# Kernel optimization log

Measured on AMD Instinct MI355X. Metric: run time of the kernel, lower is better.

The kernel has to match this reference:

```python
import jax, jax.numpy as jnp
import numpy as np

NUM_HEADS = 16
DIM = 1024
HARMONICS = 32
B, L = 2, 2048


def holo_linear(x, basis, phase, amp):
    # x: [B,L,in]; basis: [H,in] (L2-normalized rows); phase/amp: [out,H]
    # Original builds complex(res,0) * amp*exp(i*phase) and takes real of sum
    # over harmonics -> sum_h res_h * amp[o,h]*cos(phase[o,h]).
    resonance = jnp.einsum('bli,hi->blh', x, basis)        # [B,L,H]
    w = amp * jnp.cos(phase)                               # [out,H]
    return jnp.einsum('blh,oh->blo', resonance, w)         # [B,L,out]


def setup_inputs() -> dict:
    key = jax.random.key(0)
    ks = jax.random.split(key, 13)
    two_pi = 2.0 * np.pi

    def make_proj(k0, k1):
        basis = jax.random.normal(k0, (HARMONICS, DIM), dtype=jnp.float32)
        basis = basis / jnp.linalg.norm(basis, axis=1, keepdims=True)
        phase = jax.random.normal(k1, (DIM, HARMONICS), dtype=jnp.float32) * two_pi
        amp = jnp.ones((DIM, HARMONICS), dtype=jnp.float32) / HARMONICS
        return basis, phase, amp

    x = jax.random.normal(ks[0], (B, L, DIM), dtype=jnp.float32)
    bq, pq, aq = make_proj(ks[1], ks[2])
    bk, pk, ak = make_proj(ks[3], ks[4])
    bv, pv, av = make_proj(ks[5], ks[6])
    bo, po, ao = make_proj(ks[7], ks[8])
    return {
        'x': x,
        'basis_q': bq, 'phase_q': pq, 'amp_q': aq,
        'basis_k': bk, 'phase_k': pk, 'amp_k': ak,
        'basis_v': bv, 'phase_v': pv, 'amp_v': av,
        'basis_o': bo, 'phase_o': po, 'amp_o': ao,
    }


def reference(x, basis_q, phase_q, amp_q, basis_k, phase_k, amp_k,
              basis_v, phase_v, amp_v, basis_o, phase_o, amp_o):
    Bsz, Ls, C = x.shape
    head_dim = C // NUM_HEADS
    scale = head_dim ** (-0.5)

    def split_heads(t):  # [B,L,C] -> [B,H,L,hd]
        return t.reshape(Bsz, Ls, NUM_HEADS, head_dim).transpose(0, 2, 1, 3)

    q = split_heads(holo_linear(x, basis_q, phase_q, amp_q))
    k = split_heads(holo_linear(x, basis_k, phase_k, amp_k))
    v = split_heads(holo_linear(x, basis_v, phase_v, amp_v))

    attn = jnp.einsum('bhqd,bhkd->bhqk', q, k) * scale      # [B,H,L,L]
    attn = jax.nn.softmax(attn, axis=-1)
    out = jnp.einsum('bhqk,bhkd->bhqd', attn, v)            # [B,H,L,hd]
    out = out.transpose(0, 2, 1, 3).reshape(Bsz, Ls, C)
    return holo_linear(out, basis_o, phase_o, amp_o)
```

## Files before the change

### kernel.cpp

```cpp
#include <hip/hip_runtime.h>
#include <hip/hip_bf16.h>
#include <cstdint>
#include <cstddef>

#define NH   16
#define HD   64
#define CD   1024
#define HARM 32
#define BSZ  2
#define LSEQ 2048
#define NROW (BSZ*LSEQ)

typedef __attribute__((ext_vector_type(8))) short short8;
typedef __attribute__((ext_vector_type(16))) float float16v;

__device__ inline ushort bf16u(float f) {
    __hip_bfloat16 h = __float2bfloat16(f);
    return *(ushort*)&h;
}
__device__ inline float ubf(ushort u) {
    return __uint_as_float((unsigned)u << 16);
}
__device__ inline unsigned pk2(float a, float b) {
    return (unsigned)bf16u(a) | ((unsigned)bf16u(b) << 16);
}
__device__ inline int crow(int r, int half) { return (r & 3) + 8 * (r >> 2) + 4 * half; }

union S8U { short8 v; uint2 u[2]; };

__device__ inline short8 pk_frag(const unsigned* pk, int cc) {
    S8U o;
    o.u[0] = make_uint2(pk[4 * cc + 0], pk[4 * cc + 1]);
    o.u[1] = make_uint2(pk[4 * cc + 2], pk[4 * cc + 3]);
    return o.v;
}

__global__ void prep_kern(const float* __restrict__ bq, const float* __restrict__ bk,
                          const float* __restrict__ bv, const float* __restrict__ bo,
                          const float* __restrict__ pq, const float* __restrict__ aq,
                          const float* __restrict__ pk, const float* __restrict__ ak,
                          const float* __restrict__ pv, const float* __restrict__ av,
                          const float* __restrict__ po, const float* __restrict__ ao,
                          ushort* __restrict__ bF, ushort* __restrict__ wqkvF,
                          ushort* __restrict__ wobF) {
    const float QSCALE = 0.125f * 1.44269504088896340736f;
    unsigned tid = blockIdx.x * 256 + threadIdx.x;
    if (tid < 16384) {
        unsigned l31 = tid & 31, h = (tid >> 5) & 1, kc = (tid >> 6) & 63, proj = tid >> 12;
        const float* bp = (proj == 0) ? bq : (proj == 1) ? bk : (proj == 2) ? bv : bo;
        const float* s = bp + (size_t)l31 * CD + kc * 16;
        unsigned o0 = (proj == 3) ? h * 4 : h * 8;
        unsigned o1 = o0 + ((proj == 3) ? 8 : 4);
        float4 f0 = *(const float4*)(s + o0), f1 = *(const float4*)(s + o1);
        S8U o;
        o.u[0] = make_uint2(pk2(f0.x, f0.y), pk2(f0.z, f0.w));
        o.u[1] = make_uint2(pk2(f1.x, f1.y), pk2(f1.z, f1.w));
        *(short8*)(bF + (size_t)tid * 8) = o.v;
        return;
    }
    if (tid < 28672) {
        unsigned i = tid - 16384;
        unsigned l31 = i & 31, h = (i >> 5) & 1, kc2 = (i >> 6) & 1;
        unsigned ntp = (i >> 7) & 31, proj = i >> 12;
        const float* ph = (proj == 0) ? pq : (proj == 1) ? pk : pv;
        const float* am = (proj == 0) ? aq : (proj == 1) ? ak : av;
        float sc = (proj == 0) ? QSCALE : 1.0f;
        size_t s = (size_t)(ntp * 32 + l31) * HARM + kc2 * 16 + h * 4;
        float4 p0 = *(const float4*)(ph + s), p1 = *(const float4*)(ph + s + 8);
        float4 a0 = *(const float4*)(am + s), a1 = *(const float4*)(am + s + 8);
        S8U o;
        o.u[0] = make_uint2(pk2(a0.x * cosf(p0.x) * sc, a0.y * cosf(p0.y) * sc),
                            pk2(a0.z * cosf(p0.z) * sc, a0.w * cosf(p0.w) * sc));
        o.u[1] = make_uint2(pk2(a1.x * cosf(p1.x) * sc, a1.y * cosf(p1.y) * sc),
                            pk2(a1.z * cosf(p1.z) * sc, a1.w * cosf(p1.w) * sc));
        *(short8*)(wqkvF + (size_t)i * 8) = o.v;
        return;
    }
    {
        unsigned i = tid - 28672;
        unsigned l31 = i & 31, h = (i >> 5) & 1, kc2 = (i >> 6) & 1, nt = i >> 7;
        size_t s = (size_t)(nt * 32 + l31) * HARM + kc2 * 16 + h * 4;
        float4 p0 = *(const float4*)(po + s), p1 = *(const float4*)(po + s + 8);
        float4 a0 = *(const float4*)(ao + s), a1 = *(const float4*)(ao + s + 8);
        S8U o;
        o.u[0] = make_uint2(pk2(a0.x * cosf(p0.x), a0.y * cosf(p0.y)),
                            pk2(a0.z * cosf(p0.z), a0.w * cosf(p0.w)));
        o.u[1] = make_uint2(pk2(a1.x * cosf(p1.x), a1.y * cosf(p1.y)),
                            pk2(a1.z * cosf(p1.z), a1.w * cosf(p1.w)));
        *(short8*)(wobF + (size_t)i * 8) = o.v;
    }
}

__global__ __launch_bounds__(256) void res_part_kern(const float* __restrict__ x,
                                                     const ushort* __restrict__ bF,
                                                     float* __restrict__ respart) {
    __shared__ ushort xs[32 * 256];
    __shared__ float red[4 * 16 * 64];
    const int t = threadIdx.x, wave = t >> 6, lane = t & 63;
    const int l31 = lane & 31, h = lane >> 5;
    const int kseg = blockIdx.x & 3, rg = blockIdx.x >> 2;
    const int n0 = rg * 32;

#pragma unroll
    for (int i = 0; i < 8; i++) {
        int idx = i * 256 + t, row = idx >> 6, c4 = idx & 63;
        float4 v = *(const float4*)(x + (size_t)(n0 + row) * CD + kseg * 256 + c4 * 4);
        int chunk = (c4 >> 1) ^ (row & 15), sub = c4 & 1;
        *(ushort4*)(&xs[row * 256 + chunk * 8 + sub * 4]) =
            make_ushort4(bf16u(v.x), bf16u(v.y), bf16u(v.z), bf16u(v.w));
    }
    __syncthreads();

    float16v resC[3] = {};
#pragma unroll
    for (int kci = 0; kci < 4; kci++) {
        int c = wave * 8 + kci * 2 + h;
        short8 bx = *(const short8*)(&xs[l31 * 256 + (c ^ (l31 & 15)) * 8]);
        int kcg = kseg * 16 + wave * 4 + kci;
#pragma unroll
        for (int p = 0; p < 3; p++) {
            short8 a = *(const short8*)(bF + ((size_t)((p * 64 + kcg) * 2 + h) * 32 + l31) * 8);
            resC[p] = __builtin_amdgcn_mfma_f32_32x32x16_bf16(a, bx, resC[p], 0, 0, 0);
        }
    }
    float* outb = respart + ((size_t)(kseg * 128 + rg) * 3) * 1024;
    for (int p = 0; p < 3; p++) {
        __syncthreads();
#pragma unroll
        for (int r = 0; r < 16; r++) red[wave * 1024 + r * 64 + lane] = resC[p][r];
        __syncthreads();
#pragma unroll
        for (int i = 0; i < 4; i++) {
            int e = i * 256 + t;
            outb[p * 1024 + e] = (red[e] + red[1024 + e]) + (red[2048 + e] + red[3072 + e]);
        }
    }
}

__global__ __launch_bounds__(256) void rp_kern(const float* __restrict__ respart,
                                               unsigned* __restrict__ rfbuf) {
    const int tid = blockIdx.x * 256 + threadIdx.x;
    const int rest = tid / 384, u = tid % 384;
    const int p = u >> 7, cc = (u >> 6) & 1, lane = u & 63;

    const float* base = respart + ((size_t)rest * 3 + p) * 1024 + cc * 512 + lane;
    unsigned w[4];
#pragma unroll
    for (int q = 0; q < 4; q++) {
        const float* pa = base + (2 * q) * 64;
        const float* pb = pa + 64;
        float a = (pa[0] + pa[393216]) + (pa[2 * 393216] + pa[3 * 393216]);
        float bv_ = (pb[0] + pb[393216]) + (pb[2 * 393216] + pb[3 * 393216]);
        w[q] = pk2(a, bv_);
    }
    *(uint4*)(rfbuf + (size_t)rest * 1536 + ((p * 2 + cc) * 64 + lane) * 4) =
        make_uint4(w[0], w[1], w[2], w[3]);
}

__global__ __launch_bounds__(256) void qkv_kern(const unsigned* __restrict__ rfbuf,
                                                const ushort* __restrict__ wqkvF,
                                                ushort* __restrict__ qtile,
                                                ushort* __restrict__ ktile,
                                                ushort* __restrict__ vtile) {
    const int t = threadIdx.x, wave = t >> 6, lane = t & 63;
    const int l31 = lane & 31, h = lane >> 5;
    const int ntg = blockIdx.x % 24, rest = blockIdx.x / 24;
    const int b = rest >> 6, l0q = rest & 63;
    const int nt = ntg * 4 + wave;
    const int proj = nt >> 5, ntp = nt & 31;
    const int head = ntp >> 1, sub = ntp & 1;
    const int kblk = l0q >> 1, mtk = l0q & 1;

    const unsigned* rb = rfbuf + (size_t)rest * 1536 + ((proj * 2) * 64 + lane) * 4;
    uint4 q0 = *(const uint4*)(rb);
    uint4 q1 = *(const uint4*)(rb + 256);
    S8U r0, r1;
    r0.u[0] = make_uint2(q0.x, q0.y); r0.u[1] = make_uint2(q0.z, q0.w);
    r1.u[0] = make_uint2(q1.x, q1.y); r1.u[1] = make_uint2(q1.z, q1.w);

    const ushort* wp = wqkvF + ((size_t)(proj * 32 + ntp) * 4) * 256;
    short8 wf0 = *(const short8*)(wp + (size_t)h * 256 + l31 * 8);
    short8 wf1 = *(const short8*)(wp + (size_t)(2 + h) * 256 + l31 * 8);
    float16v c = {};
    if (proj < 2) {
        c = __builtin_amdgcn_mfma_f32_32x32x16_bf16(wf0, r0.v, c, 0, 0, 0);
        c = __builtin_amdgcn_mfma_f32_32x32x16_bf16(wf1, r1.v, c, 0, 0, 0);
    } else {
        c = __builtin_amdgcn_mfma_f32_32x32x16_bf16(r0.v, wf0, c, 0, 0, 0);
        c = __builtin_amdgcn_mfma_f32_32x32x16_bf16(r1.v, wf1, c, 0, 0, 0);
    }
    unsigned pkc[8];
#pragma unroll
    for (int j = 0; j < 8; j++) pkc[j] = pk2(c[2 * j], c[2 * j + 1]);

    if (proj == 0) {
        ushort* base = qtile + (((size_t)(b * NH + head) * 64 + l0q)) * 2048;
#pragma unroll
        for (int cc = 0; cc < 2; cc++)
            *(short8*)(base + (sub * 2 + cc) * 512 + h * 256 + l31 * 8) =
                pk_frag(pkc, cc);
    } else if (proj == 1) {
        ushort* base = ktile + ((size_t)(b * NH + head) * 32 + kblk) * 4096 + mtk * 2048;
#pragma unroll
        for (int cc = 0; cc < 2; cc++)
            *(short8*)(base + (sub * 2 + cc) * 512 + h * 256 + l31 * 8) =
                pk_frag(pkc, cc);
    } else {
        ushort* base = vtile + ((size_t)(b * NH + head) * 32 + kblk) * 4096 + sub * 2048;
#pragma unroll
        for (int cc = 0; cc < 2; cc++)
            *(short8*)(base + (mtk * 2 + cc) * 512 + h * 256 + l31 * 8) =
                pk_frag(pkc, cc);
    }
}

__global__ __launch_bounds__(256, 2) void flash8(const ushort* __restrict__ qtile,
                                                 const ushort* __restrict__ ktile,
                                                 const ushort* __restrict__ vtile,
                                                 ushort* __restrict__ Opart,
                                                 float* __restrict__ lbuf) {
    __shared__ ushort kb[2][4096];
    __shared__ ushort vb[2][4096];
    const int t = threadIdx.x;
    const int wave = t >> 6, lane = t & 63;
    const int l31 = lane & 31, h = lane >> 5;
    const int d = blockIdx.x;
    const int logical = (d & 7) * 128 + (d >> 3);
    const int bh = logical >> 5;
    const int inner = logical & 31;
    const int ksp = inner >> 4;
    const int qt = (inner & 15) * 4 + wave;
    const int fo = h * 256 + l31 * 8;
    const int so = t * 8;

    const ushort* qtb = qtile + ((size_t)bh * 64 + qt) * 2048;
    short8 qf[4];
#pragma unroll
    for (int kc = 0; kc < 4; kc++) qf[kc] = *(const short8*)(qtb + kc * 512 + fo);

    const ushort* ktb = ktile + (size_t)bh * 32 * 4096;
    const ushort* vtb = vtile + (size_t)bh * 32 * 4096;
    const int k0 = ksp * 16;

    {
        const ushort* ks = ktb + (size_t)k0 * 4096;
        const ushort* vs = vtb + (size_t)k0 * 4096;
        short8 a0 = *(const short8*)(ks + so);
        short8 a1 = *(const short8*)(ks + 2048 + so);
        short8 b0 = *(const short8*)(vs + so);
        short8 b1 = *(const short8*)(vs + 2048 + so);
        *(short8*)(kb[0] + so) = a0; *(short8*)(kb[0] + 2048 + so) = a1;
        *(short8*)(vb[0] + so) = b0; *(short8*)(vb[0] + 2048 + so) = b1;
    }
    __syncthreads();

    S8U ones;
    ones.u[0] = make_uint2(0x3F803F80u, 0x3F803F80u);
    ones.u[1] = make_uint2(0x3F803F80u, 0x3F803F80u);

    float16v O0 = {}, O1 = {}, La = {};

#pragma unroll
    for (int it = 0; it < 16; it++) {
        const int cur = it & 1, nxt = cur ^ 1;

        short8 a0, a1, b0, b1;
        if (it < 15) {
            const ushort* ks = ktb + (size_t)(k0 + it + 1) * 4096;
            const ushort* vs = vtb + (size_t)(k0 + it + 1) * 4096;
            a0 = *(const short8*)(ks + so);
            a1 = *(const short8*)(ks + 2048 + so);
            b0 = *(const short8*)(vs + so);
            b1 = *(const short8*)(vs + 2048 + so);
        }

        short8 kf[2][4];
#pragma unroll
        for (int mt = 0; mt < 2; mt++)
#pragma unroll
            for (int kc = 0; kc < 4; kc++)
                kf[mt][kc] = *(const short8*)(kb[cur] + mt * 2048 + kc * 512 + fo);
        float16v s0 = {}, s1 = {};
#pragma unroll
        for (int kc = 0; kc < 4; kc++) {
            s0 = __builtin_amdgcn_mfma_f32_32x32x16_bf16(kf[0][kc], qf[kc], s0, 0, 0, 0);
            s1 = __builtin_amdgcn_mfma_f32_32x32x16_bf16(kf[1][kc], qf[kc], s1, 0, 0, 0);
        }
        short8 vf[2][4];
#pragma unroll
        for (int mt = 0; mt < 2; mt++)
#pragma unroll
            for (int kc = 0; kc < 4; kc++)
                vf[mt][kc] = *(const short8*)(vb[cur] + mt * 2048 + kc * 512 + fo);

        unsigned pk0[8], pk1[8];
#pragma unroll
        for (int j2 = 0; j2 < 8; j2++) {
            pk0[j2] = pk2(__builtin_amdgcn_exp2f(s0[2 * j2]),
                          __builtin_amdgcn_exp2f(s0[2 * j2 + 1]));
            pk1[j2] = pk2(__builtin_amdgcn_exp2f(s1[2 * j2]),
                          __builtin_amdgcn_exp2f(s1[2 * j2 + 1]));
        }
#pragma unroll
        for (int kc = 0; kc < 4; kc++) {
            const unsigned* pkm = (kc < 2) ? pk0 : pk1;
            short8 bf = pk_frag(pkm, kc & 1);
            La = __builtin_amdgcn_mfma_f32_32x32x16_bf16(ones.v, bf, La, 0, 0, 0);
            O0 = __builtin_amdgcn_mfma_f32_32x32x16_bf16(vf[0][kc], bf, O0, 0, 0, 0);
            O1 = __builtin_amdgcn_mfma_f32_32x32x16_bf16(vf[1][kc], bf, O1, 0, 0, 0);
        }

        if (it < 15) {
            *(short8*)(kb[nxt] + so) = a0; *(short8*)(kb[nxt] + 2048 + so) = a1;
            *(short8*)(vb[nxt] + so) = b0; *(short8*)(vb[nxt] + 2048 + so) = b1;
        }
        __syncthreads();
    }

    if (h == 0) lbuf[(size_t)ksp * 65536 + bh * 2048 + qt * 32 + l31] = La[0];
    ushort* ob = Opart + (size_t)ksp * 4194304 + ((size_t)bh * 64 + qt) * 2048;
#pragma unroll
    for (int mt = 0; mt < 2; mt++) {
        float16v Ov = mt ? O1 : O0;
        unsigned pkO[8];
#pragma unroll
        for (int j2 = 0; j2 < 8; j2++) pkO[j2] = pk2(Ov[2 * j2], Ov[2 * j2 + 1]);
#pragma unroll
        for (int cc = 0; cc < 2; cc++)
            *(short8*)(ob + ((mt * 2 + cc) * 2 + h) * 256 + l31 * 8) =
                pk_frag(pkO, cc);
    }
}

__global__ __launch_bounds__(256) void back1_kern(const ushort* __restrict__ Opart,
                                                  const float* __restrict__ lbuf,
                                                  const ushort* __restrict__ bF,
                                                  float* __restrict__ respart2) {
    __shared__ float red[4 * 16 * 64];
    const int t = threadIdx.x, wave = t >> 6, lane = t & 63;
    const int l31 = lane & 31, h = lane >> 5;
    const int hq = blockIdx.x & 3, rg = blockIdx.x >> 2;
    const int b = rg >> 6, qt = rg & 63;
    const int hd = hq * 4 + wave, bh = b * NH + hd;

    float lb = lbuf[(size_t)bh * 2048 + qt * 32 + l31] +
               lbuf[(size_t)65536 + (size_t)bh * 2048 + qt * 32 + l31];
    float invl = 1.0f / lb;
    const ushort* ob0 = Opart + ((size_t)bh * 64 + qt) * 2048;
    const ushort* ob1 = ob0 + 4194304;

    float16v c = {};
#pragma unroll
    for (int kc = 0; kc < 4; kc++) {
        short8 o0 = *(const short8*)(ob0 + (kc * 2 + h) * 256 + l31 * 8);
        short8 o1 = *(const short8*)(ob1 + (kc * 2 + h) * 256 + l31 * 8);
        float av[8];
#pragma unroll
        for (int e = 0; e < 8; e++)
            av[e] = (ubf((ushort)o0[e]) + ubf((ushort)o1[e])) * invl;
        S8U bn;
        bn.u[0] = make_uint2(pk2(av[0], av[1]), pk2(av[2], av[3]));
        bn.u[1] = make_uint2(pk2(av[4], av[5]), pk2(av[6], av[7]));
        int kcg = hd * 4 + kc;
        short8 a = *(const short8*)(bF + ((size_t)((3 * 64 + kcg) * 2 + h) * 32 + l31) * 8);
        c = __builtin_amdgcn_mfma_f32_32x32x16_bf16(a, bn.v, c, 0, 0, 0);
    }
#pragma unroll
    for (int r = 0; r < 16; r++) red[wave * 1024 + r * 64 + lane] = c[r];
    __syncthreads();
#pragma unroll
    for (int i = 0; i < 4; i++) {
        int e = i * 256 + t;
        respart2[((size_t)hq * 128 + rg) * 1024 + e] =
            (red[e] + red[1024 + e]) + (red[2048 + e] + red[3072 + e]);
    }
}

__global__ __launch_bounds__(256) void back2_kern(const float* __restrict__ respart2,
                                                  const ushort* __restrict__ wobF,
                                                  float* __restrict__ out) {
    const int t = threadIdx.x, wave = t >> 6, lane = t & 63;
    const int l31 = lane & 31, h = lane >> 5;
    const int ng = blockIdx.x & 7, rg = blockIdx.x >> 3;

    float cf[16];
#pragma unroll
    for (int r = 0; r < 16; r++) {
        const float* pp = respart2 + r * 64 + lane;
        cf[r] = (pp[(size_t)rg * 1024] + pp[(size_t)(128 + rg) * 1024]) +
                (pp[(size_t)(256 + rg) * 1024] + pp[(size_t)(384 + rg) * 1024]);
    }
    unsigned pkr[8];
#pragma unroll
    for (int j = 0; j < 8; j++) pkr[j] = pk2(cf[2 * j], cf[2 * j + 1]);
    short8 a0 = pk_frag(pkr, 0);
    short8 a1 = pk_frag(pkr, 1);

    int nt = ng * 4 + wave;
    const ushort* wp = wobF + (size_t)nt * 1024;
    short8 wf0 = *(const short8*)(wp + (size_t)h * 256 + l31 * 8);
    short8 wf1 = *(const short8*)(wp + (size_t)(2 + h) * 256 + l31 * 8);
    float16v co = {};
    co = __builtin_amdgcn_mfma_f32_32x32x16_bf16(a0, wf0, co, 0, 0, 0);
    co = __builtin_amdgcn_mfma_f32_32x32x16_bf16(a1, wf1, co, 0, 0, 0);
#pragma unroll
    for (int r = 0; r < 16; r++) {
        int row = rg * 32 + crow(r, h);
        out[(size_t)row * CD + nt * 32 + l31] = co[r];
    }
}

extern "C" void kernel_launch(void* const* d_in, const int* in_sizes, int n_in,
                              void* d_out, int out_size, void* d_ws, size_t ws_size,
                              hipStream_t stream) {
    const float* x  = (const float*)d_in[0];
    const float* bq = (const float*)d_in[1];
    const float* pq = (const float*)d_in[2];
    const float* aq = (const float*)d_in[3];
    const float* bk = (const float*)d_in[4];
    const float* pk = (const float*)d_in[5];
    const float* ak = (const float*)d_in[6];
    const float* bv = (const float*)d_in[7];
    const float* pv = (const float*)d_in[8];
    const float* av = (const float*)d_in[9];
    const float* bo = (const float*)d_in[10];
    const float* po = (const float*)d_in[11];
    const float* ao = (const float*)d_in[12];

    char* ws = (char*)d_ws;
    ushort* bF      = (ushort*)(ws + 0);
    ushort* wqkvF   = (ushort*)(ws + 262144);
    ushort* wobF    = (ushort*)(ws + 458752);
    ushort* qtile   = (ushort*)(ws + 524288);
    ushort* ktile   = (ushort*)(ws + 8912896);
    ushort* vtile   = (ushort*)(ws + 17301504);
    ushort* Opart   = (ushort*)(ws + 25690112);
    float*  lbuf    = (float*)(ws + 42467328);
    float*  respart = (float*)(ws + 42991616);
    float*  respart2= (float*)(ws + 524288);
    unsigned* rfbuf = (unsigned*)(ws + 25690112);

    prep_kern<<<128, 256, 0, stream>>>(bq, bk, bv, bo, pq, aq, pk, ak, pv, av,
                                       po, ao, bF, wqkvF, wobF);
    res_part_kern<<<512, 256, 0, stream>>>(x, bF, respart);
    rp_kern<<<192, 256, 0, stream>>>(respart, rfbuf);
    qkv_kern<<<3072, 256, 0, stream>>>(rfbuf, wqkvF, qtile, ktile, vtile);
    flash8<<<BSZ * NH * 32, 256, 0, stream>>>(qtile, ktile, vtile, Opart, lbuf);
    back1_kern<<<512, 256, 0, stream>>>(Opart, lbuf, bF, respart2);
    back2_kern<<<1024, 256, 0, stream>>>(respart2, wobF, (float*)d_out);
}
```

Measured before the change: 158.0 us.

## Process two query tiles per wave in flash kernel to reuse K/V fragments

Each wave now handles two 32-row query tiles instead of one. The K and V fragments loaded from LDS are reused across both, and the grid is halved to 512 blocks. This is meant to cut LDS reads and K/V global loads per unit of work. In exchange it raises register pressure with doubled accumulators, which could reduce occupancy under launch_bounds(256,2), and it leaves fewer blocks to fill the CUs.

```diff
diff --git a/kernel.cpp b/kernel.cpp
--- a/kernel.cpp
+++ b/kernel.cpp
@@ -225,18 +225,22 @@
     const int wave = t >> 6, lane = t & 63;
     const int l31 = lane & 31, h = lane >> 5;
     const int d = blockIdx.x;
-    const int logical = (d & 7) * 128 + (d >> 3);
-    const int bh = logical >> 5;
-    const int inner = logical & 31;
-    const int ksp = inner >> 4;
-    const int qt = (inner & 15) * 4 + wave;
+    const int logical = (d & 7) * 64 + (d >> 3);
+    const int bh = logical >> 4;
+    const int inner = logical & 15;
+    const int ksp = inner >> 3;
+    const int qtg = inner & 7;
+    const int qt0 = qtg * 8 + wave * 2;
     const int fo = h * 256 + l31 * 8;
     const int so = t * 8;
 
-    const ushort* qtb = qtile + ((size_t)bh * 64 + qt) * 2048;
-    short8 qf[4];
-#pragma unroll
-    for (int kc = 0; kc < 4; kc++) qf[kc] = *(const short8*)(qtb + kc * 512 + fo);
+    const ushort* qtb = qtile + ((size_t)bh * 64 + qt0) * 2048;
+    short8 qfa[4], qfb[4];
+#pragma unroll
+    for (int kc = 0; kc < 4; kc++) {
+        qfa[kc] = *(const short8*)(qtb + kc * 512 + fo);
+        qfb[kc] = *(const short8*)(qtb + 2048 + kc * 512 + fo);
+    }
 
     const ushort* ktb = ktile + (size_t)bh * 32 * 4096;
     const ushort* vtb = vtile + (size_t)bh * 32 * 4096;
@@ -258,7 +262,8 @@
     ones.u[0] = make_uint2(0x3F803F80u, 0x3F803F80u);
     ones.u[1] = make_uint2(0x3F803F80u, 0x3F803F80u);
 
-    float16v O0 = {}, O1 = {}, La = {};
+    float16v O0a = {}, O1a = {}, Laa = {};
+    float16v O0b = {}, O1b = {}, Lab = {};
 
 #pragma unroll
     for (int it = 0; it < 16; it++) {
@@ -280,11 +285,13 @@
 #pragma unroll
             for (int kc = 0; kc < 4; kc++)
                 kf[mt][kc] = *(const short8*)(kb[cur] + mt * 2048 + kc * 512 + fo);
-        float16v s0 = {}, s1 = {};
+        float16v s0a = {}, s1a = {}, s0b = {}, s1b = {};
 #pragma unroll
         for (int kc = 0; kc < 4; kc++) {
-            s0 = __builtin_amdgcn_mfma_f32_32x32x16_bf16(kf[0][kc], qf[kc], s0, 0, 0, 0);
-            s1 = __builtin_amdgcn_mfma_f32_32x32x16_bf16(kf[1][kc], qf[kc], s1, 0, 0, 0);
+            s0a = __builtin_amdgcn_mfma_f32_32x32x16_bf16(kf[0][kc], qfa[kc], s0a, 0, 0, 0);
+            s1a = __builtin_amdgcn_mfma_f32_32x32x16_bf16(kf[1][kc], qfa[kc], s1a, 0, 0, 0);
+            s0b = __builtin_amdgcn_mfma_f32_32x32x16_bf16(kf[0][kc], qfb[kc], s0b, 0, 0, 0);
+            s1b = __builtin_amdgcn_mfma_f32_32x32x16_bf16(kf[1][kc], qfb[kc], s1b, 0, 0, 0);
         }
         short8 vf[2][4];
 #pragma unroll
@@ -293,21 +300,30 @@
             for (int kc = 0; kc < 4; kc++)
                 vf[mt][kc] = *(const short8*)(vb[cur] + mt * 2048 + kc * 512 + fo);
 
-        unsigned pk0[8], pk1[8];
+        unsigned pk0a[8], pk1a[8], pk0b[8], pk1b[8];
 #pragma unroll
         for (int j2 = 0; j2 < 8; j2++) {
-            pk0[j2] = pk2(__builtin_amdgcn_exp2f(s0[2 * j2]),
-                          __builtin_amdgcn_exp2f(s0[2 * j2 + 1]));
-            pk1[j2] = pk2(__builtin_amdgcn_exp2f(s1[2 * j2]),
-                          __builtin_amdgcn_exp2f(s1[2 * j2 + 1]));
+            pk0a[j2] = pk2(__builtin_amdgcn_exp2f(s0a[2 * j2]),
+                           __builtin_amdgcn_exp2f(s0a[2 * j2 + 1]));
+            pk1a[j2] = pk2(__builtin_amdgcn_exp2f(s1a[2 * j2]),
+                           __builtin_amdgcn_exp2f(s1a[2 * j2 + 1]));
+            pk0b[j2] = pk2(__builtin_amdgcn_exp2f(s0b[2 * j2]),
+                           __builtin_amdgcn_exp2f(s0b[2 * j2 + 1]));
+            pk1b[j2] = pk2(__builtin_amdgcn_exp2f(s1b[2 * j2]),
+                           __builtin_amdgcn_exp2f(s1b[2 * j2 + 1]));
         }
 #pragma unroll
         for (int kc = 0; kc < 4; kc++) {
-            const unsigned* pkm = (kc < 2) ? pk0 : pk1;
-            short8 bf = pk_frag(pkm, kc & 1);
-            La = __builtin_amdgcn_mfma_f32_32x32x16_bf16(ones.v, bf, La, 0, 0, 0);
-            O0 = __builtin_amdgcn_mfma_f32_32x32x16_bf16(vf[0][kc], bf, O0, 0, 0, 0);
-            O1 = __builtin_amdgcn_mfma_f32_32x32x16_bf16(vf[1][kc], bf, O1, 0, 0, 0);
+            const unsigned* pma = (kc < 2) ? pk0a : pk1a;
+            const unsigned* pmb = (kc < 2) ? pk0b : pk1b;
+            short8 bfa = pk_frag(pma, kc & 1);
+            short8 bfb = pk_frag(pmb, kc & 1);
+            Laa = __builtin_amdgcn_mfma_f32_32x32x16_bf16(ones.v, bfa, Laa, 0, 0, 0);
+            O0a = __builtin_amdgcn_mfma_f32_32x32x16_bf16(vf[0][kc], bfa, O0a, 0, 0, 0);
+            O1a = __builtin_amdgcn_mfma_f32_32x32x16_bf16(vf[1][kc], bfa, O1a, 0, 0, 0);
+            Lab = __builtin_amdgcn_mfma_f32_32x32x16_bf16(ones.v, bfb, Lab, 0, 0, 0);
+            O0b = __builtin_amdgcn_mfma_f32_32x32x16_bf16(vf[0][kc], bfb, O0b, 0, 0, 0);
+            O1b = __builtin_amdgcn_mfma_f32_32x32x16_bf16(vf[1][kc], bfb, O1b, 0, 0, 0);
         }
 
         if (it < 15) {
@@ -317,18 +333,24 @@
         __syncthreads();
     }
 
-    if (h == 0) lbuf[(size_t)ksp * 65536 + bh * 2048 + qt * 32 + l31] = La[0];
-    ushort* ob = Opart + (size_t)ksp * 4194304 + ((size_t)bh * 64 + qt) * 2048;
-#pragma unroll
-    for (int mt = 0; mt < 2; mt++) {
-        float16v Ov = mt ? O1 : O0;
-        unsigned pkO[8];
-#pragma unroll
-        for (int j2 = 0; j2 < 8; j2++) pkO[j2] = pk2(Ov[2 * j2], Ov[2 * j2 + 1]);
-#pragma unroll
-        for (int cc = 0; cc < 2; cc++)
-            *(short8*)(ob + ((mt * 2 + cc) * 2 + h) * 256 + l31 * 8) =
-                pk_frag(pkO, cc);
+    if (h == 0) {
+        lbuf[(size_t)ksp * 65536 + bh * 2048 + qt0 * 32 + l31] = Laa[0];
+        lbuf[(size_t)ksp * 65536 + bh * 2048 + (qt0 + 1) * 32 + l31] = Lab[0];
+    }
+#pragma unroll
+    for (int j = 0; j < 2; j++) {
+        ushort* ob = Opart + (size_t)ksp * 4194304 + ((size_t)bh * 64 + qt0 + j) * 2048;
+#pragma unroll
+        for (int mt = 0; mt < 2; mt++) {
+            float16v Ov = j ? (mt ? O1b : O0b) : (mt ? O1a : O0a);
+            unsigned pkO[8];
+#pragma unroll
+            for (int j2 = 0; j2 < 8; j2++) pkO[j2] = pk2(Ov[2 * j2], Ov[2 * j2 + 1]);
+#pragma unroll
+            for (int cc = 0; cc < 2; cc++)
+                *(short8*)(ob + ((mt * 2 + cc) * 2 + h) * 256 + l31 * 8) =
+                    pk_frag(pkO, cc);
+        }
     }
 }
 
@@ -445,7 +467,7 @@
     res_part_kern<<<512, 256, 0, stream>>>(x, bF, respart);
     rp_kern<<<192, 256, 0, stream>>>(respart, rfbuf);
     qkv_kern<<<3072, 256, 0, stream>>>(rfbuf, wqkvF, qtile, ktile, vtile);
-    flash8<<<BSZ * NH * 32, 256, 0, stream>>>(qtile, ktile, vtile, Opart, lbuf);
+    flash8<<<512, 256, 0, stream>>>(qtile, ktile, vtile, Opart, lbuf);
     back1_kern<<<512, 256, 0, stream>>>(Opart, lbuf, bF, respart2);
     back2_kern<<<1024, 256, 0, stream>>>(respart2, wobF, (float*)d_out);
 }
```

After: 151.6 us, median of 2. -4.0%, faster.

## Software-pipeline QK^T one tile ahead of exp and PV in attention loop

Applied to the files above, without the earlier changes.

Restructures the attention inner loop so the S = K·Q MFMA for the next key tile is computed while the exp/pack and P·V MFMAs of the current tile proceed. K is prefetched two tiles ahead and V one tile ahead, with separate double-buffer indices for each. This is meant to hide the exp2/pack latency behind matrix-core work and overlap more independent MFMA chains. In exchange it adds a prologue, holds two S accumulator sets in registers (more VGPR pressure), and changes the buffer-reuse pattern around the barriers.

```diff
diff --git a/kernel.cpp b/kernel.cpp
--- a/kernel.cpp
+++ b/kernel.cpp
@@ -258,49 +258,80 @@
     ones.u[0] = make_uint2(0x3F803F80u, 0x3F803F80u);
     ones.u[1] = make_uint2(0x3F803F80u, 0x3F803F80u);
 
+    float16v sS[2][2];
+    {
+        short8 ka0, ka1;
+        {
+            const ushort* ks = ktb + (size_t)(k0 + 1) * 4096;
+            ka0 = *(const short8*)(ks + so);
+            ka1 = *(const short8*)(ks + 2048 + so);
+        }
+        short8 kf[2][4];
+#pragma unroll
+        for (int mt = 0; mt < 2; mt++)
+#pragma unroll
+            for (int kc = 0; kc < 4; kc++)
+                kf[mt][kc] = *(const short8*)(kb[0] + mt * 2048 + kc * 512 + fo);
+        sS[0][0] = (float16v){};
+        sS[0][1] = (float16v){};
+#pragma unroll
+        for (int kc = 0; kc < 4; kc++) {
+            sS[0][0] = __builtin_amdgcn_mfma_f32_32x32x16_bf16(kf[0][kc], qf[kc], sS[0][0], 0, 0, 0);
+            sS[0][1] = __builtin_amdgcn_mfma_f32_32x32x16_bf16(kf[1][kc], qf[kc], sS[0][1], 0, 0, 0);
+        }
+        *(short8*)(kb[1] + so) = ka0; *(short8*)(kb[1] + 2048 + so) = ka1;
+    }
+    __syncthreads();
+
     float16v O0 = {}, O1 = {}, La = {};
 
 #pragma unroll
     for (int it = 0; it < 16; it++) {
-        const int cur = it & 1, nxt = cur ^ 1;
-
-        short8 a0, a1, b0, b1;
+        const int pc = it & 1, pn = pc ^ 1;
+
+        short8 ka0, ka1, va0, va1;
+        if (it < 14) {
+            const ushort* ks = ktb + (size_t)(k0 + it + 2) * 4096;
+            ka0 = *(const short8*)(ks + so);
+            ka1 = *(const short8*)(ks + 2048 + so);
+        }
         if (it < 15) {
-            const ushort* ks = ktb + (size_t)(k0 + it + 1) * 4096;
             const ushort* vs = vtb + (size_t)(k0 + it + 1) * 4096;
-            a0 = *(const short8*)(ks + so);
-            a1 = *(const short8*)(ks + 2048 + so);
-            b0 = *(const short8*)(vs + so);
-            b1 = *(const short8*)(vs + 2048 + so);
-        }
-
-        short8 kf[2][4];
+            va0 = *(const short8*)(vs + so);
+            va1 = *(const short8*)(vs + 2048 + so);
+        }
+
+        if (it < 15) {
+            short8 kf[2][4];
+#pragma unroll
+            for (int mt = 0; mt < 2; mt++)
+#pragma unroll
+                for (int kc = 0; kc < 4; kc++)
+                    kf[mt][kc] = *(const short8*)(kb[pn] + mt * 2048 + kc * 512 + fo);
+            sS[pn][0] = (float16v){};
+            sS[pn][1] = (float16v){};
+#pragma unroll
+            for (int kc = 0; kc < 4; kc++) {
+                sS[pn][0] = __builtin_amdgcn_mfma_f32_32x32x16_bf16(kf[0][kc], qf[kc], sS[pn][0], 0, 0, 0);
+                sS[pn][1] = __builtin_amdgcn_mfma_f32_32x32x16_bf16(kf[1][kc], qf[kc], sS[pn][1], 0, 0, 0);
+            }
+        }
+
+        unsigned pk0[8], pk1[8];
+#pragma unroll
+        for (int j2 = 0; j2 < 8; j2++) {
+            pk0[j2] = pk2(__builtin_amdgcn_exp2f(sS[pc][0][2 * j2]),
+                          __builtin_amdgcn_exp2f(sS[pc][0][2 * j2 + 1]));
+            pk1[j2] = pk2(__builtin_amdgcn_exp2f(sS[pc][1][2 * j2]),
+                          __builtin_amdgcn_exp2f(sS[pc][1][2 * j2 + 1]));
+        }
+
+        short8 vf[2][4];
 #pragma unroll
         for (int mt = 0; mt < 2; mt++)
 #pragma unroll
             for (int kc = 0; kc < 4; kc++)
-                kf[mt][kc] = *(const short8*)(kb[cur] + mt * 2048 + kc * 512 + fo);
-        float16v s0 = {}, s1 = {};
-#pragma unroll
-        for (int kc = 0; kc < 4; kc++) {
-            s0 = __builtin_amdgcn_mfma_f32_32x32x16_bf16(kf[0][kc], qf[kc], s0, 0, 0, 0);
-            s1 = __builtin_amdgcn_mfma_f32_32x32x16_bf16(kf[1][kc], qf[kc], s1, 0, 0, 0);
-        }
-        short8 vf[2][4];
-#pragma unroll
-        for (int mt = 0; mt < 2; mt++)
-#pragma unroll
-            for (int kc = 0; kc < 4; kc++)
-                vf[mt][kc] = *(const short8*)(vb[cur] + mt * 2048 + kc * 512 + fo);
-
-        unsigned pk0[8], pk1[8];
-#pragma unroll
-        for (int j2 = 0; j2 < 8; j2++) {
-            pk0[j2] = pk2(__builtin_amdgcn_exp2f(s0[2 * j2]),
-                          __builtin_amdgcn_exp2f(s0[2 * j2 + 1]));
-            pk1[j2] = pk2(__builtin_amdgcn_exp2f(s1[2 * j2]),
-                          __builtin_amdgcn_exp2f(s1[2 * j2 + 1]));
-        }
+                vf[mt][kc] = *(const short8*)(vb[pc] + mt * 2048 + kc * 512 + fo);
 #pragma unroll
         for (int kc = 0; kc < 4; kc++) {
             const unsigned* pkm = (kc < 2) ? pk0 : pk1;
@@ -310,11 +341,13 @@
             O1 = __builtin_amdgcn_mfma_f32_32x32x16_bf16(vf[1][kc], bf, O1, 0, 0, 0);
         }
 
+        if (it < 14) {
+            *(short8*)(kb[pc] + so) = ka0; *(short8*)(kb[pc] + 2048 + so) = ka1;
+        }
         if (it < 15) {
-            *(short8*)(kb[nxt] + so) = a0; *(short8*)(kb[nxt] + 2048 + so) = a1;
-            *(short8*)(vb[nxt] + so) = b0; *(short8*)(vb[nxt] + 2048 + so) = b1;
-        }
-        __syncthreads();
+            *(short8*)(vb[pn] + so) = va0; *(short8*)(vb[pn] + 2048 + so) = va1;
+            __syncthreads();
+        }
     }
 
     if (h == 0) lbuf[(size_t)ksp * 65536 + bh * 2048 + qt * 32 + l31] = La[0];
```

Measured after the change: 154.0 us. -2.5%, faster.
